# Optimization experiments

Measured on AMD Instinct MI355X. Metric: run time of the kernel, lower is better.

The kernel has to match this reference:

```python
import jax, jax.numpy as jnp
import numpy as np

R1, R2 = 0.1, 0.2  # initial_radius(0.0125) * 8, * 16
EPS = 1e-5

def sqdist(a, b):
    # a [B,N,3], b [B,M,3] -> [B,N,M]
    return jnp.sum(a * a, -1)[:, :, None] + jnp.sum(b * b, -1)[:, None, :] - 2.0 * jnp.einsum('bnc,bmc->bnm', a, b)

def gather(p, idx):
    # p [B,N,C], idx [B,...] -> [B,...,C]
    return jax.vmap(lambda pp, ii: pp[ii])(p, idx)

def fps(xyz, npoint):
    # farthest point sampling, returns int32 [B,npoint]
    B, N, _ = xyz.shape
    def step(carry, _):
        dist, far = carry
        cen = xyz[jnp.arange(B), far]                       # [B,3]
        d = jnp.sum((xyz - cen[:, None, :]) ** 2, -1)       # [B,N]
        dist = jnp.minimum(dist, d)
        nxt = jnp.argmax(dist, -1).astype(jnp.int32)
        return (dist, nxt), far
    init = (jnp.full((B, N), 1e10, xyz.dtype), jnp.zeros(B, jnp.int32))
    _, idx = jax.lax.scan(step, init, None, length=npoint)
    return idx.T

def ball_query(xyz, new_xyz, radius, nsample):
    d = sqdist(new_xyz, xyz)                                # [B,S,N]
    N = xyz.shape[1]
    cand = jnp.where(d <= radius * radius, jnp.arange(N, dtype=jnp.int32), jnp.int32(N))
    idx = -jax.lax.top_k(-cand, nsample)[0]                 # smallest nsample in-ball indices
    first = idx[..., :1]
    idx = jnp.where(idx == N, first, idx)                   # pad with first neighbor
    nearest = jnp.argmin(d, -1, keepdims=True).astype(jnp.int32)
    return jnp.where(idx == N, nearest, idx)                # fallback if ball empty

def bn_relu(x, g, b, axes):
    # training-mode batchnorm (biased var) + relu, channel-last
    m = jnp.mean(x, axes, keepdims=True)
    v = jnp.mean((x - m) ** 2, axes, keepdims=True)
    return jax.nn.relu((x - m) * jax.lax.rsqrt(v + EPS) * g + b)

def set_abstraction(xyz, feat, npoint, radius, nsample, layers):
    new_xyz = gather(xyz, fps(xyz, npoint))                 # [B,S,3]
    gidx = ball_query(xyz, new_xyz, radius, nsample)        # [B,S,K]
    gx = gather(xyz, gidx) - new_xyz[:, :, None, :]         # [B,S,K,3]
    h = jnp.concatenate([gx, gather(feat, gidx)], -1)       # [B,S,K,3+C]
    for w, g, b in layers:
        h = bn_relu(jnp.einsum('bskc,oc->bsko', h, w), g, b, (0, 1, 2))
    return new_xyz, jnp.max(h, 2)                           # [B,S,Cout]

def set_upconv(pos1, pos2, feat1, feat2, nsample, w1, g1, b1, w2, g2, b2):
    idx = jax.lax.top_k(-sqdist(pos1, pos2), nsample)[1]    # knn into sparse cloud [B,N,K]
    gp = gather(pos2, idx) - pos1[:, :, None, :]
    h = jnp.concatenate([gather(feat2, idx), gp], -1)       # [B,N,K,C2+3]
    h = bn_relu(jnp.einsum('bnkc,oc->bnko', h, w1), g1, b1, (0, 1, 2))
    h = jnp.max(h, 2)
    h = jnp.concatenate([h, feat1], -1)                     # [B,N,mlp[-1]+C1]
    return bn_relu(jnp.einsum('bnc,oc->bno', h, w2), g2, b2, (0, 1))

def feature_prop(pos1, pos2, feat1, feat2, w, g, b):
    negd, idx = jax.lax.top_k(-sqdist(pos1, pos2), 3)       # 3-NN
    dist = jnp.maximum(-negd, 1e-10)
    wgt = 1.0 / dist
    wgt = wgt / jnp.sum(wgt, -1, keepdims=True)
    interp = jnp.sum(gather(feat2, idx) * wgt[..., None], 2)
    h = jnp.concatenate([interp, feat1], -1)
    return bn_relu(jnp.einsum('bnc,oc->bno', h, w), g, b, (0, 1))

def _forward(points1, fea1, points2, fea2,
             sa1_w0, sa1_g0, sa1_b0, sa1_w1, sa1_g1, sa1_b1,
             sa2_w0, sa2_g0, sa2_b0, sa2_w1, sa2_g1, sa2_b1,
             su1_w1, su1_g1, su1_b1, su1_w2, su1_g2, su1_b2,
             fp_w, fp_g, fp_b, bn1_g, bn1_b, conv2_w, conv2_b):
    def pipeline(pts, fea):
        l1x, l1f = set_abstraction(pts, fea, 4096, R1, 16,
                                   [(sa1_w0, sa1_g0, sa1_b0), (sa1_w1, sa1_g1, sa1_b1)])
        l2x, l2f = set_abstraction(l1x, l1f, 1024, R2, 16,
                                   [(sa2_w0, sa2_g0, sa2_b0), (sa2_w1, sa2_g1, sa2_b1)])
        l1n = set_upconv(l1x, l2x, l1f, l2f, 8, su1_w1, su1_g1, su1_b1, su1_w2, su1_g2, su1_b2)
        l0n = feature_prop(pts, l1x, fea, l1n, fp_w, fp_g, fp_b)
        x = bn_relu(l0n, bn1_g, bn1_b, (0, 1))              # relu(bn1(.))
        sf = jnp.einsum('bnc,oc->bno', x, conv2_w) + conv2_b
        return jnp.concatenate([pts, sf], -1)               # include_pos
    return jnp.stack([pipeline(points1, fea1), pipeline(points2, fea2)])  # [2,B,N,19]

def setup_inputs() -> dict:
    key = jax.random.key(0)
    ks = jax.random.split(key, 12)
    B, N, C = 2, 8192, 10
    def w(k, o, i):
        return jax.random.normal(k, (o, i), jnp.float32) * 0.1
    inp = {
        'points1': jax.random.uniform(ks[0], (B, N, 3), jnp.float32),
        'fea1': jax.random.normal(ks[1], (B, N, C), jnp.float32),
        'points2': jax.random.uniform(ks[2], (B, N, 3), jnp.float32),
        'fea2': jax.random.normal(ks[3], (B, N, C), jnp.float32),
        'sa1_w0': w(ks[4], 16, 13), 'sa1_g0': jnp.ones(16), 'sa1_b0': jnp.zeros(16),
        'sa1_w1': w(ks[5], 32, 16), 'sa1_g1': jnp.ones(32), 'sa1_b1': jnp.zeros(32),
        'sa2_w0': w(ks[6], 32, 35), 'sa2_g0': jnp.ones(32), 'sa2_b0': jnp.zeros(32),
        'sa2_w1': w(ks[7], 64, 32), 'sa2_g1': jnp.ones(64), 'sa2_b1': jnp.zeros(64),
        'su1_w1': w(ks[8], 32, 67), 'su1_g1': jnp.ones(32), 'su1_b1': jnp.zeros(32),
        'su1_w2': w(ks[9], 32, 64), 'su1_g2': jnp.ones(32), 'su1_b2': jnp.zeros(32),
        'fp_w': w(ks[10], 32, 42), 'fp_g': jnp.ones(32), 'fp_b': jnp.zeros(32),
        'bn1_g': jnp.ones(32), 'bn1_b': jnp.zeros(32),
        'conv2_w': w(ks[11], 16, 32), 'conv2_b': jnp.zeros(16),
    }
    return inp

def reference(points1, fea1, points2, fea2,
              sa1_w0, sa1_g0, sa1_b0, sa1_w1, sa1_g1, sa1_b1,
              sa2_w0, sa2_g0, sa2_b0, sa2_w1, sa2_g1, sa2_b1,
              su1_w1, su1_g1, su1_b1, su1_w2, su1_g2, su1_b2,
              fp_w, fp_g, fp_b, bn1_g, bn1_b, conv2_w, conv2_b):
    return _forward(points1, fea1, points2, fea2,
                    sa1_w0, sa1_g0, sa1_b0, sa1_w1, sa1_g1, sa1_b1,
                    sa2_w0, sa2_g0, sa2_b0, sa2_w1, sa2_g1, sa2_b1,
                    su1_w1, su1_g1, su1_b1, su1_w2, su1_g2, su1_b2,
                    fp_w, fp_g, fp_b, bn1_g, bn1_b, conv2_w, conv2_b)
```

## Files before the change

kernel.cpp:

```cpp
#include <hip/hip_runtime.h>

#define DI __device__ __forceinline__

enum : int {
  OFF_XYZF = 0,
  OFF_FEAF = OFF_XYZF + 4*8192*3,
  OFF_NX1  = OFF_FEAF + 4*8192*10,
  OFF_L1F  = OFF_NX1  + 4*4096*3,
  OFF_NX2  = OFF_L1F  + 4*4096*32,
  OFF_L2F  = OFF_NX2  + 4*1024*3,
  OFF_UH2  = OFF_L2F  + 4*1024*64,
  OFF_L1N  = OFF_UH2  + 4*4096*32,
  OFF_H3   = OFF_L1N  + 4*4096*32,
  OFF_L0N  = OFF_H3   + 4*8192*32,
  OFF_STATS= OFF_L0N  + 4*8192*32,
  OFF_GIDX1= OFF_STATS + 2048,
  OFF_GIDX2= OFF_GIDX1 + 4*4096*16,
  OFF_UIDX = OFF_GIDX2 + 4*1024*16,
  WS_END   = OFF_UIDX + 4*4096*8
};
enum : int { ST_SA1A=0, ST_SA1B=64, ST_SA2A=128, ST_SA2B=192, ST_U1=320, ST_U2=384, ST_FP=448, ST_BN1=512 };

DI float nrm3(float x, float y, float z){ return fmaf(z,z, fmaf(y,y, x*x)); }
DI float dot3(float ax,float ay,float az,float bx,float by,float bz){
  return fmaf(az,bz, fmaf(ay,by, ax*bx));
}

template<int CTRL>
DI float dpp_fmax(float v){
  int o = __builtin_amdgcn_update_dpp(0, __float_as_int(v), CTRL, 0xf, 0xf, true);
  return fmaxf(v, __int_as_float(o));
}
template<int CTRL>
DI int dpp_imin(int v){
  int o = __builtin_amdgcn_update_dpp(0x7fffffff, v, CTRL, 0xf, 0xf, true);
  return v < o ? v : o;
}
DI float wave_fmax(float v){
  v = dpp_fmax<0xB1>(v);
  v = dpp_fmax<0x4E>(v);
  v = dpp_fmax<0x141>(v);
  v = dpp_fmax<0x140>(v);
  v = fmaxf(v, __int_as_float(__builtin_amdgcn_ds_swizzle(__float_as_int(v), 0x401F)));
  v = fmaxf(v, __shfl_xor(v, 32, 64));
  return v;
}
DI int wave_imin(int v){
  v = dpp_imin<0xB1>(v);
  v = dpp_imin<0x4E>(v);
  v = dpp_imin<0x141>(v);
  v = dpp_imin<0x140>(v);
  { int o = __builtin_amdgcn_ds_swizzle(v, 0x401F); v = v<o?v:o; }
  { int o = __shfl_xor(v, 32, 64);                  v = v<o?v:o; }
  return v;
}

template<int CH>
DI void stats_accum(float* h, float* dst, float (*sred)[128])
{
  float sq[CH];
  #pragma unroll
  for (int c=0;c<CH;c++) sq[c]=h[c]*h[c];
  #pragma unroll
  for (int m=1;m<64;m<<=1){
    #pragma unroll
    for (int c=0;c<CH;c++){ h[c] += __shfl_xor(h[c], m, 64); sq[c] += __shfl_xor(sq[c], m, 64); }
  }
  const int tid=threadIdx.x, wid=tid>>6, lane=tid&63;
  if (lane==0){
    #pragma unroll
    for (int c=0;c<CH;c++){ sred[wid][c]=h[c]; sred[wid][CH+c]=sq[c]; }
  }
  __syncthreads();
  if (tid < 2*CH){
    float v = sred[0][tid]+sred[1][tid]+sred[2][tid]+sred[3][tid];
    atomicAdd(dst+tid, v);
  }
}

__global__ __launch_bounds__(256) void prep(const float* __restrict__ p1,const float* __restrict__ f1,
                                            const float* __restrict__ p2,const float* __restrict__ f2,
                                            float* __restrict__ xyzf, float* __restrict__ feaf)
{
  const int i = blockIdx.x*256+threadIdx.x;
  const int z = i>>13, n = i&8191, pipe=z>>1, b=z&1;
  const float* ps = (pipe?p2:p1) + (b*8192+n)*3;
  const float* fs = (pipe?f2:f1) + (b*8192+n)*10;
  float* xo = xyzf + (z*8192+n)*3;
  float* fo = feaf + (z*8192+n)*10;
  #pragma unroll
  for (int c=0;c<3;c++)  xo[c]=ps[c];
  #pragma unroll
  for (int c=0;c<10;c++) fo[c]=fs[c];
}

template<int N,int NPOINT,int T>
__global__ __launch_bounds__(T) void fps_kernel(const float* __restrict__ src, float* __restrict__ dst)
{
  constexpr int P = N/T;
  const int z = blockIdx.x;
  const float* xyz = src + z*N*3;
  float* nx = dst + z*NPOINT*3;
  const int t = threadIdx.x;
  __shared__ float sx[N], sy[N], szz[N];
  __shared__ unsigned long long s_acc[3];
  float px[P],py[P],pz[P],dist[P];
  #pragma unroll
  for (int k=0;k<P;k++){
    const int j = t + k*T;
    float x=xyz[j*3+0], y=xyz[j*3+1], w=xyz[j*3+2];
    px[k]=x; py[k]=y; pz[k]=w; dist[k]=1e10f;
    sx[j]=x; sy[j]=y; szz[j]=w;
  }
  if (t==0){ s_acc[0]=0ull; s_acc[1]=0ull; s_acc[2]=0ull; }
  __syncthreads();
  unsigned long long win = (unsigned long long)(unsigned)(N-1);
  for (int s=0;;s++){
    const int cur = (N-1) - (int)(unsigned)(win & 0xffffffffull);
    if (t==0){ nx[s*3+0]=sx[cur]; nx[s*3+1]=sy[cur]; nx[s*3+2]=szz[cur]; }
    if (s == NPOINT-1) break;
    const float cx=sx[cur], cy=sy[cur], cz=szz[cur];
    float lm = -1.0f;
    #pragma unroll
    for (int k=0;k<P;k+=2){
      float dx0=px[k]-cx,   dy0=py[k]-cy,   dz0=pz[k]-cz;
      float dx1=px[k+1]-cx, dy1=py[k+1]-cy, dz1=pz[k+1]-cz;
      float d0 = fmaf(dz0,dz0, fmaf(dy0,dy0, dx0*dx0));
      float d1 = fmaf(dz1,dz1, fmaf(dy1,dy1, dx1*dx1));
      float n0 = fminf(dist[k],   d0);
      float n1 = fminf(dist[k+1], d1);
      dist[k]=n0; dist[k+1]=n1;
      lm = fmaxf(lm, fmaxf(n0,n1));
    }
    int kb = 0;
    #pragma unroll
    for (int k=P-1;k>=0;k--) if (dist[k]==lm) kb = k;
    const float wm = wave_fmax(lm);
    int jc = (lm==wm) ? (t + kb*T) : 0x7fffffff;
    jc = wave_imin(jc);
    if ((t&63)==0)
      atomicMax(&s_acc[s%3], ((unsigned long long)__float_as_uint(wm)<<32)
                           | (unsigned long long)(unsigned)(N-1-jc));
    if (t==0) s_acc[(s+1)%3] = 0ull;
    __syncthreads();
    win = s_acc[s%3];
  }
}

template<int NSRC,int SQ,int K>
__global__ __launch_bounds__(64) void ball_query(const float* __restrict__ qxyz, const float* __restrict__ sxyz,
                                                 int* __restrict__ gidx, float r2)
{
  __shared__ float4 tile[1024];
  const int z = blockIdx.y, tid = threadIdx.x;
  const int s = blockIdx.x*64 + tid;
  const float* q = qxyz + (z*SQ+s)*3;
  const float qx=q[0],qy=q[1],qz=q[2];
  const float qq=nrm3(qx,qy,qz);
  int cnt=0, first=0, amin=0; float dmin=3.0e38f;
  int* out = gidx + (z*SQ+s)*K;
  for (int t0=0;t0<NSRC;t0+=1024){
    __syncthreads();
    for (int i=tid;i<1024;i+=64){
      const float* p = sxyz + (z*NSRC+t0+i)*3;
      float x=p[0],y=p[1],w=p[2];
      tile[i]=make_float4(x,y,w,nrm3(x,y,w));
    }
    __syncthreads();
    for (int jj=0;jj<1024;jj++){
      float4 p = tile[jj];
      float dot=dot3(qx,qy,qz,p.x,p.y,p.z);
      float d=(qq+p.w)-2.0f*dot;
      const int j = t0+jj;
      if (d < dmin){ dmin=d; amin=j; }
      if (d <= r2 && cnt < K){ if(cnt==0) first=j; out[cnt]=j; cnt++; }
    }
  }
  const int fill = (cnt==0)? amin : first;
  for (int c=cnt;c<K;c++) out[c]=fill;
}

template<int S,int K,int CF,int C1,int C2,int NSRC,int PASS>
__global__ __launch_bounds__(256) void sa_pass(
    const float* __restrict__ srcxyz, const float* __restrict__ srcfea,
    const float* __restrict__ qxyz, const int* __restrict__ gidx,
    const float* __restrict__ w0, const float* __restrict__ g0, const float* __restrict__ b0,
    const float* __restrict__ w1, const float* __restrict__ g1v, const float* __restrict__ b1v,
    float* __restrict__ stats, int offA, int offB, float cnt0, float cnt1,
    float* __restrict__ outp)
{
  constexpr int CIN = 3+CF;
  __shared__ float w0l[C1*CIN];
  __shared__ float w1l[PASS>=2 ? C2*C1 : 1];
  __shared__ float sc0[C1], bi0[C1];
  __shared__ float sc1[C2], bi1[C2];
  __shared__ float sred[4][128];
  const int z = blockIdx.y, pipe = z>>1, tid = threadIdx.x;
  float* stA = stats + pipe*1024 + offA;
  float* stB = stats + pipe*1024 + offB;
  for (int i=tid;i<C1*CIN;i+=256) w0l[i]=w0[i];
  if (PASS>=2){
    for (int i=tid;i<C2*C1;i+=256) w1l[i]=w1[i];
    if (tid<C1){
      float m = stA[tid]/cnt0;
      float var = stA[C1+tid]/cnt0 - m*m;
      float rs = 1.0f/sqrtf(var+1e-5f);
      float sc = rs*g0[tid];
      sc0[tid]=sc; bi0[tid]=b0[tid]-m*sc;
    }
  }
  if (PASS==3 && tid<C2){
    float m = stB[tid]/cnt1;
    float var = stB[C2+tid]/cnt1 - m*m;
    float rs = 1.0f/sqrtf(var+1e-5f);
    float sc = rs*g1v[tid];
    sc1[tid]=sc; bi1[tid]=b1v[tid]-m*sc;
  }
  __syncthreads();
  const int item = blockIdx.x*256+tid;
  const int s = item/K;
  const int j = gidx[(z*S+s)*K + (item%K)];
  const float* q = qxyz + (z*S+s)*3;
  const float* p = srcxyz + (z*NSRC+j)*3;
  float f[CIN];
  f[0]=p[0]-q[0]; f[1]=p[1]-q[1]; f[2]=p[2]-q[2];
  const float* fe = srcfea + (z*NSRC+j)*CF;
  #pragma unroll
  for (int c=0;c<CF;c++) f[3+c]=fe[c];
  float h1[C1];
  #pragma unroll
  for (int o=0;o<C1;o++){
    float a=0.f;
    #pragma unroll
    for (int c=0;c<CIN;c++) a = fmaf(w0l[o*CIN+c], f[c], a);
    h1[o]=a;
  }
  if (PASS==1){ stats_accum<C1>(h1, stA, sred); return; }
  float f2v[C1];
  #pragma unroll
  for (int o=0;o<C1;o++) f2v[o]=fmaxf(fmaf(h1[o],sc0[o],bi0[o]), 0.f);
  float h2[C2];
  #pragma unroll
  for (int o=0;o<C2;o++){
    float a=0.f;
    #pragma unroll
    for (int c=0;c<C1;c++) a = fmaf(w1l[o*C1+c], f2v[c], a);
    h2[o]=a;
  }
  if (PASS==2){ stats_accum<C2>(h2, stB, sred); return; }
  #pragma unroll
  for (int o=0;o<C2;o++) h2[o]=fmaxf(fmaf(h2[o],sc1[o],bi1[o]), 0.f);
  #pragma unroll
  for (int msk=1; msk<K; msk<<=1){
    #pragma unroll
    for (int o=0;o<C2;o++) h2[o]=fmaxf(h2[o], __shfl_xor(h2[o], msk, 64));
  }
  if ((tid & (K-1))==0){
    float* op = outp + (z*S+s)*C2;
    #pragma unroll
    for (int o=0;o<C2;o++) op[o]=h2[o];
  }
}

__global__ __launch_bounds__(64) void up_top8(const float* __restrict__ nx1, const float* __restrict__ nx2,
                                              int* __restrict__ uidx)
{
  __shared__ float4 tile[1024];
  const int z=blockIdx.y, tid=threadIdx.x;
  const int s=blockIdx.x*64+tid;
  const float* q = nx1 + (z*4096+s)*3;
  const float qx=q[0],qy=q[1],qz=q[2];
  const float qq=nrm3(qx,qy,qz);
  for (int i=tid;i<1024;i+=64){
    const float* p = nx2 + (z*1024+i)*3;
    float x=p[0],y=p[1],w=p[2];
    tile[i]=make_float4(x,y,w,nrm3(x,y,w));
  }
  __syncthreads();
  float d[8]; int id[8];
  #pragma unroll
  for (int r=0;r<8;r++){ d[r]=3e38f; id[r]=0; }
  for (int j=0;j<1024;j++){
    float4 p=tile[j];
    float dt=dot3(qx,qy,qz,p.x,p.y,p.z);
    float dd=(qq+p.w)-2.0f*dt;
    if (dd<d[7]){
      d[7]=dd; id[7]=j;
      #pragma unroll
      for (int r=7;r>0;r--){
        if (d[r]<d[r-1]){ float td=d[r-1]; d[r-1]=d[r]; d[r]=td; int ti=id[r-1]; id[r-1]=id[r]; id[r]=ti; }
      }
    }
  }
  int* o = uidx + (z*4096+s)*8;
  #pragma unroll
  for (int r=0;r<8;r++) o[r]=id[r];
}

template<int PASS>
__global__ __launch_bounds__(256) void up_pass(
    const float* __restrict__ nx1, const float* __restrict__ nx2,
    const float* __restrict__ l2f, const float* __restrict__ l1f,
    const int* __restrict__ uidx,
    const float* __restrict__ w1, const float* __restrict__ g1v, const float* __restrict__ b1v,
    const float* __restrict__ w2,
    float* __restrict__ stats, float* __restrict__ uh2)
{
  __shared__ float w1l[32*67];
  __shared__ float w2l[PASS==2?32*64:1];
  __shared__ float sc0[32], bi0[32];
  __shared__ float sred[4][128];
  const int z=blockIdx.y, pipe=z>>1, tid=threadIdx.x;
  float* stU1 = stats + pipe*1024 + ST_U1;
  float* stU2 = stats + pipe*1024 + ST_U2;
  for (int i=tid;i<32*67;i+=256) w1l[i]=w1[i];
  if (PASS==2){
    for (int i=tid;i<32*64;i+=256) w2l[i]=w2[i];
    if (tid<32){
      float m=stU1[tid]/65536.f;
      float var=stU1[32+tid]/65536.f - m*m;
      float rs=1.0f/sqrtf(var+1e-5f);
      float sc=rs*g1v[tid];
      sc0[tid]=sc; bi0[tid]=b1v[tid]-m*sc;
    }
  }
  __syncthreads();
  const int item = blockIdx.x*256+tid;
  const int s = item>>3, k = item&7;
  const int j = uidx[(z*4096+s)*8+k];
  float f67[67];
  const float* fe = l2f + (z*1024+j)*64;
  #pragma unroll
  for (int c=0;c<64;c++) f67[c]=fe[c];
  const float* pp = nx2 + (z*1024+j)*3;
  const float* qv = nx1 + (z*4096+s)*3;
  f67[64]=pp[0]-qv[0]; f67[65]=pp[1]-qv[1]; f67[66]=pp[2]-qv[2];
  float h[32];
  #pragma unroll
  for (int o=0;o<32;o++){
    float a=0.f;
    #pragma unroll
    for (int c=0;c<67;c++) a=fmaf(w1l[o*67+c], f67[c], a);
    h[o]=a;
  }
  if (PASS==1){ stats_accum<32>(h, stU1, sred); return; }
  #pragma unroll
  for (int o=0;o<32;o++) h[o]=fmaxf(fmaf(h[o],sc0[o],bi0[o]),0.f);
  #pragma unroll
  for (int msk=1; msk<8; msk<<=1){
    #pragma unroll
    for (int o=0;o<32;o++) h[o]=fmaxf(h[o], __shfl_xor(h[o],msk,64));
  }
  float h2[32];
  if (k==0){
    const float* l1 = l1f + (z*4096+s)*32;
    #pragma unroll
    for (int o=0;o<32;o++){
      float a=0.f;
      #pragma unroll
      for (int c=0;c<32;c++) a=fmaf(w2l[o*64+c], h[c], a);
      #pragma unroll
      for (int c=0;c<32;c++) a=fmaf(w2l[o*64+32+c], l1[c], a);
      h2[o]=a;
    }
    float* up = uh2 + (z*4096+s)*32;
    #pragma unroll
    for (int o=0;o<32;o++) up[o]=h2[o];
  } else {
    #pragma unroll
    for (int o=0;o<32;o++) h2[o]=0.f;
  }
  stats_accum<32>(h2, stU2, sred);
}

__global__ __launch_bounds__(256) void up_norm(const float* __restrict__ uh2, const float* __restrict__ g,
                                               const float* __restrict__ b, const float* __restrict__ stats,
                                               float* __restrict__ l1n)
{
  const int i = blockIdx.x*256+threadIdx.x;
  const int z = i>>17, pipe = z>>1, c = i&31;
  const float* st = stats + pipe*1024 + ST_U2;
  float m = st[c]/8192.f;
  float var = st[32+c]/8192.f - m*m;
  float rs = 1.0f/sqrtf(var+1e-5f);
  float sc = rs*g[c];
  float bi = b[c]-m*sc;
  l1n[i]=fmaxf(fmaf(uh2[i],sc,bi),0.f);
}

__global__ __launch_bounds__(256) void fp_kern(
  const float* __restrict__ xyzf, const float* __restrict__ feaf,
  const float* __restrict__ nx1, const float* __restrict__ l1n,
  const float* __restrict__ fpw, float* __restrict__ stats, float* __restrict__ h3)
{
  __shared__ float4 tile[2048];
  __shared__ float wl[32*42];
  __shared__ float sred[4][128];
  const int z=blockIdx.y, pipe=z>>1, tid=threadIdx.x;
  for (int i=tid;i<32*42;i+=256) wl[i]=fpw[i];
  const int n = blockIdx.x*256+tid;
  const float* q = xyzf + (z*8192+n)*3;
  const float qx=q[0],qy=q[1],qz=q[2];
  const float qq2=nrm3(qx,qy,qz);
  float d0=3e38f,d1=3e38f,d2=3e38f; int i0=0,i1=0,i2=0;
  for (int t0=0;t0<4096;t0+=2048){
    __syncthreads();
    for (int i=tid;i<2048;i+=256){
      const float* p = nx1 + (z*4096+t0+i)*3;
      float x=p[0],y=p[1],w=p[2];
      tile[i]=make_float4(x,y,w,nrm3(x,y,w));
    }
    __syncthreads();
    for (int jj=0;jj<2048;jj++){
      float4 p=tile[jj];
      float dt=dot3(qx,qy,qz,p.x,p.y,p.z);
      float d=(qq2+p.w)-2.0f*dt;
      if (d<d2){
        d2=d; i2=t0+jj;
        if (d2<d1){ float td=d1; d1=d2; d2=td; int ti=i1; i1=i2; i2=ti; }
        if (d1<d0){ float td=d0; d0=d1; d1=td; int ti=i0; i0=i1; i1=ti; }
      }
    }
  }
  d0=fmaxf(d0,1e-10f); d1=fmaxf(d1,1e-10f); d2=fmaxf(d2,1e-10f);
  float w0=1.0f/d0, w1=1.0f/d1, w2=1.0f/d2;
  float wsum=(w0+w1)+w2;
  w0/=wsum; w1/=wsum; w2/=wsum;
  const float* A = l1n + (z*4096+i0)*32;
  const float* B = l1n + (z*4096+i1)*32;
  const float* C = l1n + (z*4096+i2)*32;
  float f[42];
  #pragma unroll
  for (int c=0;c<32;c++) f[c]=fmaf(C[c],w2, fmaf(B[c],w1, A[c]*w0));
  const float* fe = feaf + (z*8192+n)*10;
  #pragma unroll
  for (int c=0;c<10;c++) f[32+c]=fe[c];
  float h[32];
  #pragma unroll
  for (int o=0;o<32;o++){
    float a=0.f;
    #pragma unroll
    for (int c=0;c<42;c++) a=fmaf(wl[o*42+c], f[c], a);
    h[o]=a;
    h3[(z*8192+n)*32+o]=a;
  }
  stats_accum<32>(h, stats + pipe*1024 + ST_FP, sred);
}

__global__ __launch_bounds__(256) void fp_post(const float* __restrict__ h3, const float* __restrict__ g,
                                               const float* __restrict__ b, float* __restrict__ stats,
                                               float* __restrict__ l0n)
{
  __shared__ float sc[32], bi[32];
  __shared__ float sred[4][128];
  const int tid=threadIdx.x;
  const int row = blockIdx.x*256+tid;
  const int pipe = row>>14;
  float* stF = stats + pipe*1024 + ST_FP;
  float* stB = stats + pipe*1024 + ST_BN1;
  if (tid<32){
    float m=stF[tid]/16384.f;
    float var=stF[32+tid]/16384.f-m*m;
    float rs=1.0f/sqrtf(var+1e-5f);
    float s=rs*g[tid];
    sc[tid]=s; bi[tid]=b[tid]-m*s;
  }
  __syncthreads();
  float x[32];
  #pragma unroll
  for (int c=0;c<32;c++){ x[c]=fmaxf(fmaf(h3[row*32+c],sc[c],bi[c]),0.f); l0n[row*32+c]=x[c]; }
  stats_accum<32>(x, stB, sred);
}

__global__ __launch_bounds__(256) void final_kern(
  const float* __restrict__ l0n, const float* __restrict__ g, const float* __restrict__ b,
  const float* __restrict__ cw, const float* __restrict__ cb,
  const float* __restrict__ p1, const float* __restrict__ p2,
  const float* __restrict__ stats, float* __restrict__ out)
{
  __shared__ float sc[32], bi[32], wl[512], bl[16];
  const int tid=threadIdx.x;
  const int row = blockIdx.x*256+tid;
  const int z=row>>13, pipe=z>>1, bb=z&1, n=row&8191;
  const float* st = stats + pipe*1024 + ST_BN1;
  if (tid<32){
    float m=st[tid]/16384.f;
    float var=st[32+tid]/16384.f-m*m;
    float rs=1.0f/sqrtf(var+1e-5f);
    float s=rs*g[tid];
    sc[tid]=s; bi[tid]=b[tid]-m*s;
  }
  for (int i=tid;i<512;i+=256) wl[i]=cw[i];
  if (tid<16) bl[tid]=cb[tid];
  __syncthreads();
  float x[32];
  #pragma unroll
  for (int c=0;c<32;c++) x[c]=fmaxf(fmaf(l0n[row*32+c],sc[c],bi[c]),0.f);
  float* o = out + row*19;
  const float* ps = (pipe?p2:p1) + (bb*8192+n)*3;
  o[0]=ps[0]; o[1]=ps[1]; o[2]=ps[2];
  #pragma unroll
  for (int oo=0;oo<16;oo++){
    float a=0.f;
    #pragma unroll
    for (int c=0;c<32;c++) a=fmaf(wl[oo*32+c],x[c],a);
    o[3+oo]=a+bl[oo];
  }
}

extern "C" void kernel_launch(void* const* d_in, const int* in_sizes, int n_in,
                              void* d_out, int out_size, void* d_ws, size_t ws_size,
                              hipStream_t stream)
{
  (void)in_sizes; (void)n_in; (void)out_size; (void)ws_size;
  const float* p1 = (const float*)d_in[0];
  const float* f1 = (const float*)d_in[1];
  const float* p2 = (const float*)d_in[2];
  const float* f2 = (const float*)d_in[3];
  const float *sa1_w0=(const float*)d_in[4], *sa1_g0=(const float*)d_in[5], *sa1_b0=(const float*)d_in[6];
  const float *sa1_w1=(const float*)d_in[7], *sa1_g1=(const float*)d_in[8], *sa1_b1=(const float*)d_in[9];
  const float *sa2_w0=(const float*)d_in[10],*sa2_g0=(const float*)d_in[11],*sa2_b0=(const float*)d_in[12];
  const float *sa2_w1=(const float*)d_in[13],*sa2_g1=(const float*)d_in[14],*sa2_b1=(const float*)d_in[15];
  const float *su1_w1=(const float*)d_in[16],*su1_g1=(const float*)d_in[17],*su1_b1=(const float*)d_in[18];
  const float *su1_w2=(const float*)d_in[19],*su1_g2=(const float*)d_in[20],*su1_b2=(const float*)d_in[21];
  const float *fp_w=(const float*)d_in[22], *fp_g=(const float*)d_in[23], *fp_b=(const float*)d_in[24];
  const float *bn1_g=(const float*)d_in[25],*bn1_b=(const float*)d_in[26];
  const float *conv2_w=(const float*)d_in[27],*conv2_b=(const float*)d_in[28];
  float* wsf=(float*)d_ws; int* wsi=(int*)d_ws;
  float* xyzf=wsf+OFF_XYZF; float* feaf=wsf+OFF_FEAF;
  float* nx1=wsf+OFF_NX1; float* l1f=wsf+OFF_L1F;
  float* nx2=wsf+OFF_NX2; float* l2f=wsf+OFF_L2F;
  float* uh2=wsf+OFF_UH2; float* l1n=wsf+OFF_L1N;
  float* h3=wsf+OFF_H3; float* l0n=wsf+OFF_L0N;
  float* stats=wsf+OFF_STATS;
  int* gidx1=wsi+OFF_GIDX1; int* gidx2=wsi+OFF_GIDX2; int* uidx=wsi+OFF_UIDX;
  const float R2A=(float)(0.1*0.1), R2B=(float)(0.2*0.2);

  (void)hipMemsetAsync(stats, 0, 2048*sizeof(float), stream);
  prep<<<128,256,0,stream>>>(p1,f1,p2,f2,xyzf,feaf);
  fps_kernel<8192,4096,512><<<4,512,0,stream>>>(xyzf, nx1);
  ball_query<8192,4096,16><<<dim3(64,4),64,0,stream>>>(nx1, xyzf, gidx1, R2A);
  sa_pass<4096,16,10,16,32,8192,1><<<dim3(256,4),256,0,stream>>>(xyzf,feaf,nx1,gidx1,
      sa1_w0,sa1_g0,sa1_b0,sa1_w1,sa1_g1,sa1_b1, stats,ST_SA1A,ST_SA1B,131072.f,131072.f, l1f);
  sa_pass<4096,16,10,16,32,8192,2><<<dim3(256,4),256,0,stream>>>(xyzf,feaf,nx1,gidx1,
      sa1_w0,sa1_g0,sa1_b0,sa1_w1,sa1_g1,sa1_b1, stats,ST_SA1A,ST_SA1B,131072.f,131072.f, l1f);
  sa_pass<4096,16,10,16,32,8192,3><<<dim3(256,4),256,0,stream>>>(xyzf,feaf,nx1,gidx1,
      sa1_w0,sa1_g0,sa1_b0,sa1_w1,sa1_g1,sa1_b1, stats,ST_SA1A,ST_SA1B,131072.f,131072.f, l1f);
  fps_kernel<4096,1024,512><<<4,512,0,stream>>>(nx1, nx2);
  ball_query<4096,1024,16><<<dim3(16,4),64,0,stream>>>(nx2, nx1, gidx2, R2B);
  sa_pass<1024,16,32,32,64,4096,1><<<dim3(64,4),256,0,stream>>>(nx1,l1f,nx2,gidx2,
      sa2_w0,sa2_g0,sa2_b0,sa2_w1,sa2_g1,sa2_b1, stats,ST_SA2A,ST_SA2B,32768.f,32768.f, l2f);
  sa_pass<1024,16,32,32,64,4096,2><<<dim3(64,4),256,0,stream>>>(nx1,l1f,nx2,gidx2,
      sa2_w0,sa2_g0,sa2_b0,sa2_w1,sa2_g1,sa2_b1, stats,ST_SA2A,ST_SA2B,32768.f,32768.f, l2f);
  sa_pass<1024,16,32,32,64,4096,3><<<dim3(64,4),256,0,stream>>>(nx1,l1f,nx2,gidx2,
      sa2_w0,sa2_g0,sa2_b0,sa2_w1,sa2_g1,sa2_b1, stats,ST_SA2A,ST_SA2B,32768.f,32768.f, l2f);
  up_top8<<<dim3(64,4),64,0,stream>>>(nx1,nx2,uidx);
  up_pass<1><<<dim3(128,4),256,0,stream>>>(nx1,nx2,l2f,l1f,uidx,su1_w1,su1_g1,su1_b1,su1_w2,stats,uh2);
  up_pass<2><<<dim3(128,4),256,0,stream>>>(nx1,nx2,l2f,l1f,uidx,su1_w1,su1_g1,su1_b1,su1_w2,stats,uh2);
  up_norm<<<2048,256,0,stream>>>(uh2,su1_g2,su1_b2,stats,l1n);
  fp_kern<<<dim3(32,4),256,0,stream>>>(xyzf,feaf,nx1,l1n,fp_w,stats,h3);
  fp_post<<<128,256,0,stream>>>(h3,fp_g,fp_b,stats,l0n);
  final_kern<<<128,256,0,stream>>>(l0n,bn1_g,bn1_b,conv2_w,conv2_b,p1,p2,stats,(float*)d_out);
}
```

Before: 5.818 ms.

## Rewrite farthest point sampling with spatial buckets and bounding-box pruning

Replaces the FPS kernel with one that first sorts points into Morton-ordered 8x8x8 spatial cells. Each wave then owns contiguous 64-point buckets, and the kernel keeps a per-bucket bounding box, max-distance key and argmax coordinate in shared memory. At each step it picks the winner from the bucket keys and updates only buckets whose box lower bound could beat their current max distance. This aims to cut the per-iteration distance and reduction work of the long sequential FPS loop. In exchange it adds setup cost (histogram, scan and scatter), more shared-memory traffic and divergent reductions per bucket.

New measurement: 8.538 ms. +46.8%, slower.

```diff
diff --git a/kernel.cpp b/kernel.cpp
--- a/kernel.cpp
+++ b/kernel.cpp
@@ -32,9 +32,19 @@
   return fmaxf(v, __int_as_float(o));
 }
 template<int CTRL>
+DI float dpp_fmin(float v){
+  int o = __builtin_amdgcn_update_dpp(0, __float_as_int(v), CTRL, 0xf, 0xf, true);
+  return fminf(v, __int_as_float(o));
+}
+template<int CTRL>
 DI int dpp_imin(int v){
   int o = __builtin_amdgcn_update_dpp(0x7fffffff, v, CTRL, 0xf, 0xf, true);
   return v < o ? v : o;
+}
+template<int CTRL>
+DI int dpp_imax(int v){
+  int o = __builtin_amdgcn_update_dpp((int)0x80000000, v, CTRL, 0xf, 0xf, true);
+  return v > o ? v : o;
 }
 DI float wave_fmax(float v){
   v = dpp_fmax<0xB1>(v);
@@ -45,6 +55,15 @@
   v = fmaxf(v, __shfl_xor(v, 32, 64));
   return v;
 }
+DI float wave_fmin(float v){
+  v = dpp_fmin<0xB1>(v);
+  v = dpp_fmin<0x4E>(v);
+  v = dpp_fmin<0x141>(v);
+  v = dpp_fmin<0x140>(v);
+  v = fminf(v, __int_as_float(__builtin_amdgcn_ds_swizzle(__float_as_int(v), 0x401F)));
+  v = fminf(v, __shfl_xor(v, 32, 64));
+  return v;
+}
 DI int wave_imin(int v){
   v = dpp_imin<0xB1>(v);
   v = dpp_imin<0x4E>(v);
@@ -54,6 +73,15 @@
   { int o = __shfl_xor(v, 32, 64);                  v = v<o?v:o; }
   return v;
 }
+DI int wave_imax(int v){
+  v = dpp_imax<0xB1>(v);
+  v = dpp_imax<0x4E>(v);
+  v = dpp_imax<0x141>(v);
+  v = dpp_imax<0x140>(v);
+  { int o = __builtin_amdgcn_ds_swizzle(v, 0x401F); v = v>o?v:o; }
+  { int o = __shfl_xor(v, 32, 64);                  v = v>o?v:o; }
+  return v;
+}
 
 template<int CH>
 DI void stats_accum(float* h, float* dst, float (*sred)[128])
@@ -94,56 +122,129 @@
   for (int c=0;c<10;c++) fo[c]=fs[c];
 }
 
-template<int N,int NPOINT,int T>
-__global__ __launch_bounds__(T) void fps_kernel(const float* __restrict__ src, float* __restrict__ dst)
-{
-  constexpr int P = N/T;
+DI int mspread(int v){ return (v&1) | ((v&2)<<2) | ((v&4)<<4); }
+
+template<int N,int NPOINT>
+__global__ __launch_bounds__(512) void fps_bucket(const float* __restrict__ src, float* __restrict__ dst)
+{
+  constexpr int T=512, NW=8, NB=N/64, KB=NB/NW, P=N/T, KPL=NB/64;
+  static_assert(P==KB, "slot count must equal points-per-lane");
   const int z = blockIdx.x;
   const float* xyz = src + z*N*3;
   float* nx = dst + z*NPOINT*3;
-  const int t = threadIdx.x;
-  __shared__ float sx[N], sy[N], szz[N];
-  __shared__ unsigned long long s_acc[3];
-  float px[P],py[P],pz[P],dist[P];
+  const int t = threadIdx.x, w = t>>6, lane = t&63;
+
+  __shared__ int hist[512], offs[512], wsum[8];
+  __shared__ int sidx[N];
+  __shared__ unsigned long long gk[2][NB];
+  __shared__ float4 wx4[2][NB];
+
+  hist[t]=0;
+  __syncthreads();
+  int code_[P];
+  #pragma unroll
+  for (int i=0;i<P;i++){
+    const int j = t + i*T;
+    float x=xyz[j*3], y=xyz[j*3+1], zz=xyz[j*3+2];
+    int a=(int)(x*8.f);  a=a<0?0:(a>7?7:a);
+    int b=(int)(y*8.f);  b=b<0?0:(b>7?7:b);
+    int c=(int)(zz*8.f); c=c<0?0:(c>7?7:c);
+    int mc = mspread(a) | (mspread(b)<<1) | (mspread(c)<<2);
+    code_[i]=mc;
+    atomicAdd(&hist[mc],1);
+  }
+  __syncthreads();
+  {
+    int x = hist[t];
+    int ix = x;
+    #pragma unroll
+    for (int m=1;m<64;m<<=1){ int y=__shfl_up(ix,m,64); if (lane>=m) ix+=y; }
+    if (lane==63) wsum[w]=ix;
+    __syncthreads();
+    int base=0;
+    #pragma unroll
+    for (int q=0;q<NW-1;q++) base += (q<w)? wsum[q] : 0;
+    offs[t] = base + ix - x;
+  }
+  __syncthreads();
+  #pragma unroll
+  for (int i=0;i<P;i++){
+    int pos = atomicAdd(&offs[code_[i]],1);
+    sidx[pos] = t + i*T;
+  }
+  __syncthreads();
+  float px[P],py[P],pz[P],dist[P]; int oi[P];
   #pragma unroll
   for (int k=0;k<P;k++){
-    const int j = t + k*T;
-    float x=xyz[j*3+0], y=xyz[j*3+1], w=xyz[j*3+2];
-    px[k]=x; py[k]=y; pz[k]=w; dist[k]=1e10f;
-    sx[j]=x; sy[j]=y; szz[j]=w;
-  }
-  if (t==0){ s_acc[0]=0ull; s_acc[1]=0ull; s_acc[2]=0ull; }
-  __syncthreads();
-  unsigned long long win = (unsigned long long)(unsigned)(N-1);
+    const int sp = (k*NW+w)*64 + lane;
+    const int j = sidx[sp];
+    oi[k]=j;
+    px[k]=xyz[j*3]; py[k]=xyz[j*3+1]; pz[k]=xyz[j*3+2];
+    dist[k]=1e10f;
+  }
+  float blox=0.f,bloy=0.f,bloz=0.f,bhix=0.f,bhiy=0.f,bhiz=0.f;
+  unsigned long long mykey=0ull;
+  #pragma unroll
+  for (int k=0;k<P;k++){
+    const int b = k*NW+w;
+    float lx=wave_fmin(px[k]), hx=wave_fmax(px[k]);
+    float ly=wave_fmin(py[k]), hy=wave_fmax(py[k]);
+    float lz=wave_fmin(pz[k]), hz=wave_fmax(pz[k]);
+    int jm = wave_imin(oi[k]);
+    unsigned long long key = ((unsigned long long)__float_as_uint(1e10f)<<32)
+                           | (unsigned)(N-1-jm);
+    if (oi[k]==jm) wx4[0][b] = make_float4(px[k],py[k],pz[k],0.f);
+    if (lane==0)   gk[0][b]  = key;
+    if (lane==k){ blox=lx;bhix=hx;bloy=ly;bhiy=hy;bloz=lz;bhiz=hz; mykey=key; }
+  }
+  __syncthreads();
   for (int s=0;;s++){
-    const int cur = (N-1) - (int)(unsigned)(win & 0xffffffffull);
-    if (t==0){ nx[s*3+0]=sx[cur]; nx[s*3+1]=sy[cur]; nx[s*3+2]=szz[cur]; }
-    if (s == NPOINT-1) break;
-    const float cx=sx[cur], cy=sy[cur], cz=szz[cur];
-    float lm = -1.0f;
-    #pragma unroll
-    for (int k=0;k<P;k+=2){
-      float dx0=px[k]-cx,   dy0=py[k]-cy,   dz0=pz[k]-cz;
-      float dx1=px[k+1]-cx, dy1=py[k+1]-cy, dz1=pz[k+1]-cz;
-      float d0 = fmaf(dz0,dz0, fmaf(dy0,dy0, dx0*dx0));
-      float d1 = fmaf(dz1,dz1, fmaf(dy1,dy1, dx1*dx1));
-      float n0 = fminf(dist[k],   d0);
-      float n1 = fminf(dist[k+1], d1);
-      dist[k]=n0; dist[k+1]=n1;
-      lm = fmaxf(lm, fmaxf(n0,n1));
-    }
-    int kb = 0;
-    #pragma unroll
-    for (int k=P-1;k>=0;k--) if (dist[k]==lm) kb = k;
-    const float wm = wave_fmax(lm);
-    int jc = (lm==wm) ? (t + kb*T) : 0x7fffffff;
-    jc = wave_imin(jc);
-    if ((t&63)==0)
-      atomicMax(&s_acc[s%3], ((unsigned long long)__float_as_uint(wm)<<32)
-                           | (unsigned long long)(unsigned)(N-1-jc));
-    if (t==0) s_acc[(s+1)%3] = 0ull;
+    const int cur=s&1, nxt=cur^1;
+    unsigned long long k0 = gk[cur][lane*KPL];
+    unsigned long long k1 = (KPL==2) ? gk[cur][lane*KPL+1] : k0;
+    float v0 = __uint_as_float((unsigned)(k0>>32));
+    float v1 = __uint_as_float((unsigned)(k1>>32));
+    float wm = wave_fmax(fmaxf(v0,v1));
+    int c0 = (v0==wm)? (int)(unsigned)(k0 & 0xffffffffull) : -1;
+    int c1 = (v1==wm)? (int)(unsigned)(k1 & 0xffffffffull) : -1;
+    int em = wave_imax(c0>c1?c0:c1);
+    bool hh = (c0==em)||(c1==em);
+    unsigned long long bal = __ballot(hh);
+    int fl = __ffsll((long long)bal)-1;
+    int which = __shfl((c0==em)?0:1, fl, 64);
+    int bid = fl*KPL + which;
+    float4 wc = wx4[cur][bid];
+    if (t==0){ nx[s*3]=wc.x; nx[s*3+1]=wc.y; nx[s*3+2]=wc.z; }
+    if (s==NPOINT-1) break;
+    const float cx=wc.x, cy=wc.y, cz=wc.z;
+    if (lane<KB) wx4[nxt][lane*NW+w] = wx4[cur][lane*NW+w];
+    float dxm = fmaxf(fmaxf(blox-cx, cx-bhix), 0.f);
+    float dym = fmaxf(fmaxf(bloy-cy, cy-bhiy), 0.f);
+    float dzm = fmaxf(fmaxf(bloz-cz, cz-bhiz), 0.f);
+    float lb  = fmaf(dzm,dzm, fmaf(dym,dym, dxm*dxm));
+    float ub  = __uint_as_float((unsigned)(mykey>>32));
+    bool sf = (lane<KB) && (lb*0.99999f < ub);
+    unsigned mlo = (unsigned)__ballot(sf);
+    mlo = __builtin_amdgcn_readfirstlane(mlo);
+    #pragma unroll
+    for (int k=0;k<P;k++){
+      if (mlo & (1u<<k)){
+        const int b = k*NW+w;
+        float dx=px[k]-cx, dy=py[k]-cy, dz=pz[k]-cz;
+        float d  = fmaf(dz,dz, fmaf(dy,dy, dx*dx));
+        float nd = fminf(dist[k], d);
+        dist[k]=nd;
+        float bm = wave_fmax(nd);
+        int jc = (nd==bm)? oi[k] : 0x7fffffff;
+        int jm = wave_imin(jc);
+        unsigned long long key = ((unsigned long long)__float_as_uint(bm)<<32)
+                               | (unsigned)(N-1-jm);
+        if (jc==jm) wx4[nxt][b] = make_float4(px[k],py[k],pz[k],0.f);
+        if (lane==k) mykey = key;
+      }
+    }
+    if (lane<KB) gk[nxt][lane*NW+w] = mykey;
     __syncthreads();
-    win = s_acc[s%3];
   }
 }
 
@@ -538,7 +639,7 @@
 
   (void)hipMemsetAsync(stats, 0, 2048*sizeof(float), stream);
   prep<<<128,256,0,stream>>>(p1,f1,p2,f2,xyzf,feaf);
-  fps_kernel<8192,4096,512><<<4,512,0,stream>>>(xyzf, nx1);
+  fps_bucket<8192,4096><<<4,512,0,stream>>>(xyzf, nx1);
   ball_query<8192,4096,16><<<dim3(64,4),64,0,stream>>>(nx1, xyzf, gidx1, R2A);
   sa_pass<4096,16,10,16,32,8192,1><<<dim3(256,4),256,0,stream>>>(xyzf,feaf,nx1,gidx1,
       sa1_w0,sa1_g0,sa1_b0,sa1_w1,sa1_g1,sa1_b1, stats,ST_SA1A,ST_SA1B,131072.f,131072.f, l1f);
@@ -546,7 +647,7 @@
       sa1_w0,sa1_g0,sa1_b0,sa1_w1,sa1_g1,sa1_b1, stats,ST_SA1A,ST_SA1B,131072.f,131072.f, l1f);
   sa_pass<4096,16,10,16,32,8192,3><<<dim3(256,4),256,0,stream>>>(xyzf,feaf,nx1,gidx1,
       sa1_w0,sa1_g0,sa1_b0,sa1_w1,sa1_g1,sa1_b1, stats,ST_SA1A,ST_SA1B,131072.f,131072.f, l1f);
-  fps_kernel<4096,1024,512><<<4,512,0,stream>>>(nx1, nx2);
+  fps_bucket<4096,1024><<<4,512,0,stream>>>(nx1, nx2);
   ball_query<4096,1024,16><<<dim3(16,4),64,0,stream>>>(nx2, nx1, gidx2, R2B);
   sa_pass<1024,16,32,32,64,4096,1><<<dim3(64,4),256,0,stream>>>(nx1,l1f,nx2,gidx2,
       sa2_w0,sa2_g0,sa2_b0,sa2_w1,sa2_g1,sa2_b1, stats,ST_SA2A,ST_SA2B,32768.f,32768.f, l2f);
```

## Spatially bin FPS points per thread and skip updates via bounding-box bound

Applied to the files above, without the earlier changes.

Farthest point sampling now sorts points into Morton-ordered voxel cells with a shared histogram and prefix sum, so each thread owns a spatially compact group of points. Each thread keeps a bounding box and skips its distance update when the box's lower-bound distance to the new centroid cannot lower its current max. The wave reductions are changed to row_shr/row_bcast DPP sequences read from lane 63, and the cross-wave argmax becomes per-wave slots scanned by every thread instead of 64-bit atomics. This cuts the serial per-iteration arithmetic and atomic traffic in FPS. In exchange it adds setup sorting, extra shared memory, warp divergence, and a bounding-box skip test with a slack factor whose exactness must be preserved.

Measured after the change: 6.792 ms. 16.7% more time.

```diff
diff --git a/kernel.cpp b/kernel.cpp
--- a/kernel.cpp
+++ b/kernel.cpp
@@ -27,31 +27,31 @@
 }
 
 template<int CTRL>
-DI float dpp_fmax(float v){
+DI float dppmax_f(float v){
   int o = __builtin_amdgcn_update_dpp(0, __float_as_int(v), CTRL, 0xf, 0xf, true);
   return fmaxf(v, __int_as_float(o));
 }
 template<int CTRL>
-DI int dpp_imin(int v){
-  int o = __builtin_amdgcn_update_dpp(0x7fffffff, v, CTRL, 0xf, 0xf, true);
+DI int dppmin_i(int v){
+  int o = __builtin_amdgcn_update_dpp(0x7fffffff, v, CTRL, 0xf, 0xf, false);
   return v < o ? v : o;
 }
-DI float wave_fmax(float v){
-  v = dpp_fmax<0xB1>(v);
-  v = dpp_fmax<0x4E>(v);
-  v = dpp_fmax<0x141>(v);
-  v = dpp_fmax<0x140>(v);
-  v = fmaxf(v, __int_as_float(__builtin_amdgcn_ds_swizzle(__float_as_int(v), 0x401F)));
-  v = fmaxf(v, __shfl_xor(v, 32, 64));
+DI float red63_fmax(float v){
+  v = dppmax_f<0x111>(v);
+  v = dppmax_f<0x112>(v);
+  v = dppmax_f<0x114>(v);
+  v = dppmax_f<0x118>(v);
+  v = dppmax_f<0x142>(v);
+  v = dppmax_f<0x143>(v);
   return v;
 }
-DI int wave_imin(int v){
-  v = dpp_imin<0xB1>(v);
-  v = dpp_imin<0x4E>(v);
-  v = dpp_imin<0x141>(v);
-  v = dpp_imin<0x140>(v);
-  { int o = __builtin_amdgcn_ds_swizzle(v, 0x401F); v = v<o?v:o; }
-  { int o = __shfl_xor(v, 32, 64);                  v = v<o?v:o; }
+DI int red63_imin(int v){
+  v = dppmin_i<0x111>(v);
+  v = dppmin_i<0x112>(v);
+  v = dppmin_i<0x114>(v);
+  v = dppmin_i<0x118>(v);
+  v = dppmin_i<0x142>(v);
+  v = dppmin_i<0x143>(v);
   return v;
 }
 
@@ -94,56 +94,119 @@
   for (int c=0;c<10;c++) fo[c]=fs[c];
 }
 
-template<int N,int NPOINT,int T>
-__global__ __launch_bounds__(T) void fps_kernel(const float* __restrict__ src, float* __restrict__ dst)
-{
-  constexpr int P = N/T;
+DI int mspread(int v){ return (v&1) | ((v&2)<<2) | ((v&4)<<4); }
+
+template<int N,int NPOINT>
+__global__ __launch_bounds__(512) void fps_lane(const float* __restrict__ src, float* __restrict__ dst)
+{
+  constexpr int T=512, P=N/T;
   const int z = blockIdx.x;
   const float* xyz = src + z*N*3;
   float* nx = dst + z*NPOINT*3;
-  const int t = threadIdx.x;
+  const int t = threadIdx.x, w = t>>6, lane = t&63;
+
   __shared__ float sx[N], sy[N], szz[N];
-  __shared__ unsigned long long s_acc[3];
-  float px[P],py[P],pz[P],dist[P];
+  __shared__ int hist[512], offs[512], wsum[8];
+  __shared__ int sidx[N];
+  __shared__ unsigned long long s_wk[2][8];
+
+  hist[t]=0;
+  __syncthreads();
+  int code_[P];
+  #pragma unroll
+  for (int i=0;i<P;i++){
+    const int j = t + i*T;
+    float x=xyz[j*3], y=xyz[j*3+1], zz=xyz[j*3+2];
+    sx[j]=x; sy[j]=y; szz[j]=zz;
+    int a=(int)(x*8.f);  a=a<0?0:(a>7?7:a);
+    int b=(int)(y*8.f);  b=b<0?0:(b>7?7:b);
+    int c=(int)(zz*8.f); c=c<0?0:(c>7?7:c);
+    int mc = mspread(a) | (mspread(b)<<1) | (mspread(c)<<2);
+    code_[i]=mc;
+    atomicAdd(&hist[mc],1);
+  }
+  __syncthreads();
+  {
+    int x = hist[t];
+    int ix = x;
+    #pragma unroll
+    for (int m=1;m<64;m<<=1){ int y=__shfl_up(ix,m,64); if (lane>=m) ix+=y; }
+    if (lane==63) wsum[w]=ix;
+    __syncthreads();
+    int base=0;
+    #pragma unroll
+    for (int q=0;q<7;q++) base += (q<w)? wsum[q] : 0;
+    offs[t] = base + ix - x;
+  }
+  __syncthreads();
+  #pragma unroll
+  for (int i=0;i<P;i++){
+    int pos = atomicAdd(&offs[code_[i]],1);
+    sidx[pos] = t + i*T;
+  }
+  __syncthreads();
+  float px[P],py[P],pz[P],dist[P]; int oi[P];
   #pragma unroll
   for (int k=0;k<P;k++){
-    const int j = t + k*T;
-    float x=xyz[j*3+0], y=xyz[j*3+1], w=xyz[j*3+2];
-    px[k]=x; py[k]=y; pz[k]=w; dist[k]=1e10f;
-    sx[j]=x; sy[j]=y; szz[j]=w;
-  }
-  if (t==0){ s_acc[0]=0ull; s_acc[1]=0ull; s_acc[2]=0ull; }
-  __syncthreads();
-  unsigned long long win = (unsigned long long)(unsigned)(N-1);
+    const int j = sidx[t*P+k];
+    oi[k]=j;
+    px[k]=sx[j]; py[k]=sy[j]; pz[k]=szz[j];
+    dist[k]=1e10f;
+  }
+  float blox=px[0],bhix=px[0],bloy=py[0],bhiy=py[0],bloz=pz[0],bhiz=pz[0];
+  int jb = oi[0];
+  #pragma unroll
+  for (int k=1;k<P;k++){
+    blox=fminf(blox,px[k]); bhix=fmaxf(bhix,px[k]);
+    bloy=fminf(bloy,py[k]); bhiy=fmaxf(bhiy,py[k]);
+    bloz=fminf(bloz,pz[k]); bhiz=fmaxf(bhiz,pz[k]);
+    jb = oi[k]<jb ? oi[k] : jb;
+  }
+  float lm = 1e10f;
+
   for (int s=0;;s++){
-    const int cur = (N-1) - (int)(unsigned)(win & 0xffffffffull);
-    if (t==0){ nx[s*3+0]=sx[cur]; nx[s*3+1]=sy[cur]; nx[s*3+2]=szz[cur]; }
-    if (s == NPOINT-1) break;
+    float wmv = red63_fmax(lm);
+    float swm = __int_as_float(__builtin_amdgcn_readlane(__float_as_int(wmv), 63));
+    int jc = (lm==swm) ? jb : 0x7fffffff;
+    int jcv = red63_imin(jc);
+    int sjw = __builtin_amdgcn_readlane(jcv, 63);
+    if (lane==0)
+      s_wk[s&1][w] = ((unsigned long long)__float_as_uint(swm)<<32)
+                   | (unsigned)(N-1-sjw);
+    __syncthreads();
+    unsigned long long bk = s_wk[s&1][0];
+    #pragma unroll
+    for (int q=1;q<8;q++){ unsigned long long o=s_wk[s&1][q]; bk = o>bk?o:bk; }
+    const int cur = (N-1) - (int)(unsigned)(bk & 0xffffffffull);
+    if (t==0){ nx[s*3]=sx[cur]; nx[s*3+1]=sy[cur]; nx[s*3+2]=szz[cur]; }
+    if (s==NPOINT-1) break;
     const float cx=sx[cur], cy=sy[cur], cz=szz[cur];
-    float lm = -1.0f;
-    #pragma unroll
-    for (int k=0;k<P;k+=2){
-      float dx0=px[k]-cx,   dy0=py[k]-cy,   dz0=pz[k]-cz;
-      float dx1=px[k+1]-cx, dy1=py[k+1]-cy, dz1=pz[k+1]-cz;
-      float d0 = fmaf(dz0,dz0, fmaf(dy0,dy0, dx0*dx0));
-      float d1 = fmaf(dz1,dz1, fmaf(dy1,dy1, dx1*dx1));
-      float n0 = fminf(dist[k],   d0);
-      float n1 = fminf(dist[k+1], d1);
-      dist[k]=n0; dist[k+1]=n1;
-      lm = fmaxf(lm, fmaxf(n0,n1));
-    }
-    int kb = 0;
-    #pragma unroll
-    for (int k=P-1;k>=0;k--) if (dist[k]==lm) kb = k;
-    const float wm = wave_fmax(lm);
-    int jc = (lm==wm) ? (t + kb*T) : 0x7fffffff;
-    jc = wave_imin(jc);
-    if ((t&63)==0)
-      atomicMax(&s_acc[s%3], ((unsigned long long)__float_as_uint(wm)<<32)
-                           | (unsigned long long)(unsigned)(N-1-jc));
-    if (t==0) s_acc[(s+1)%3] = 0ull;
-    __syncthreads();
-    win = s_acc[s%3];
+    float dxm = fmaxf(fmaxf(blox-cx, cx-bhix), 0.f);
+    float dym = fmaxf(fmaxf(bloy-cy, cy-bhiy), 0.f);
+    float dzm = fmaxf(fmaxf(bloz-cz, cz-bhiz), 0.f);
+    float lb  = fmaf(dzm,dzm, fmaf(dym,dym, dxm*dxm));
+    if (lb*0.99999f < lm){
+      float a=-1.f, b2=-1.f;
+      #pragma unroll
+      for (int k=0;k<P;k+=2){
+        float dx0=px[k]-cx,   dy0=py[k]-cy,   dz0=pz[k]-cz;
+        float dx1=px[k+1]-cx, dy1=py[k+1]-cy, dz1=pz[k+1]-cz;
+        float d0 = fmaf(dz0,dz0, fmaf(dy0,dy0, dx0*dx0));
+        float d1 = fmaf(dz1,dz1, fmaf(dy1,dy1, dx1*dx1));
+        float n0 = fminf(dist[k],   d0);
+        float n1 = fminf(dist[k+1], d1);
+        dist[k]=n0; dist[k+1]=n1;
+        a=fmaxf(a,n0); b2=fmaxf(b2,n1);
+      }
+      lm = fmaxf(a,b2);
+      int nj = 0x7fffffff;
+      #pragma unroll
+      for (int k=0;k<P;k++){
+        int cand = (dist[k]==lm) ? oi[k] : 0x7fffffff;
+        nj = cand<nj ? cand : nj;
+      }
+      jb = nj;
+    }
   }
 }
 
@@ -538,7 +601,7 @@
 
   (void)hipMemsetAsync(stats, 0, 2048*sizeof(float), stream);
   prep<<<128,256,0,stream>>>(p1,f1,p2,f2,xyzf,feaf);
-  fps_kernel<8192,4096,512><<<4,512,0,stream>>>(xyzf, nx1);
+  fps_lane<8192,4096><<<4,512,0,stream>>>(xyzf, nx1);
   ball_query<8192,4096,16><<<dim3(64,4),64,0,stream>>>(nx1, xyzf, gidx1, R2A);
   sa_pass<4096,16,10,16,32,8192,1><<<dim3(256,4),256,0,stream>>>(xyzf,feaf,nx1,gidx1,
       sa1_w0,sa1_g0,sa1_b0,sa1_w1,sa1_g1,sa1_b1, stats,ST_SA1A,ST_SA1B,131072.f,131072.f, l1f);
@@ -546,7 +609,7 @@
       sa1_w0,sa1_g0,sa1_b0,sa1_w1,sa1_g1,sa1_b1, stats,ST_SA1A,ST_SA1B,131072.f,131072.f, l1f);
   sa_pass<4096,16,10,16,32,8192,3><<<dim3(256,4),256,0,stream>>>(xyzf,feaf,nx1,gidx1,
       sa1_w0,sa1_g0,sa1_b0,sa1_w1,sa1_g1,sa1_b1, stats,ST_SA1A,ST_SA1B,131072.f,131072.f, l1f);
-  fps_kernel<4096,1024,512><<<4,512,0,stream>>>(nx1, nx2);
+  fps_lane<4096,1024><<<4,512,0,stream>>>(nx1, nx2);
   ball_query<4096,1024,16><<<dim3(16,4),64,0,stream>>>(nx2, nx1, gidx2, R2B);
   sa_pass<1024,16,32,32,64,4096,1><<<dim3(64,4),256,0,stream>>>(nx1,l1f,nx2,gidx2,
       sa2_w0,sa2_g0,sa2_b0,sa2_w1,sa2_g1,sa2_b1, stats,ST_SA2A,ST_SA2B,32768.f,32768.f, l2f);
```
